# Performance work log

Hardware: AMD Instinct MI355X
Metric: run time of the kernel (lower is better)

Reference implementation:

```python
import jax, jax.numpy as jnp
import numpy as np


def _gcn_layer(x, row, col, W, b):
    # x: [N, d_in]; row/col: [E'] (with self loops already appended)
    N = x.shape[0]
    deg = jax.ops.segment_sum(jnp.ones_like(row, dtype=x.dtype), row, num_segments=N)
    deg_inv_sqrt = deg ** -0.5  # self loops guarantee deg >= 1
    norm = deg_inv_sqrt[row] * deg_inv_sqrt[col]  # [E']
    msg = norm[:, None] * x[row]                  # gather + normalize
    aggr = jax.ops.segment_sum(msg, col, num_segments=N)  # scatter-add
    return aggr @ W + b


def reference(x, edge_index, W1, b1, W2, b2):
    N = x.shape[0]
    loops = jnp.arange(N, dtype=edge_index.dtype)
    row = jnp.concatenate([edge_index[0], loops])
    col = jnp.concatenate([edge_index[1], loops])
    h = jax.nn.relu(_gcn_layer(x, row, col, W1, b1))
    # F.dropout(training=self.training) is identity in eval mode
    out = _gcn_layer(h, row, col, W2, b2)
    return jax.nn.log_softmax(out, axis=1)


def setup_inputs() -> dict:
    key = jax.random.key(0)
    k1, k2, k3, k4 = jax.random.split(key, 4)
    N, E, F_IN, F_HID, F_OUT = 100000, 1200000, 64, 64, 16
    x = jax.random.normal(k1, (N, F_IN), dtype=jnp.float32)
    edge_index = jax.random.randint(k2, (2, E), 0, N, dtype=jnp.int64)
    W1 = jax.random.normal(k3, (F_IN, F_HID), dtype=jnp.float32) / np.sqrt(F_IN)
    b1 = jnp.zeros((F_HID,), dtype=jnp.float32)
    W2 = jax.random.normal(k4, (F_HID, F_OUT), dtype=jnp.float32) / np.sqrt(F_HID)
    b2 = jnp.zeros((F_OUT,), dtype=jnp.float32)
    return {"x": x, "edge_index": edge_index, "W1": W1, "b1": b1, "W2": W2, "b2": b2}
```

## Files before the change

### kernel.cpp

```cpp
#include <hip/hip_runtime.h>
#include <hip/hip_bf16.h>

typedef __attribute__((ext_vector_type(8))) _Float16 hfrag;
typedef __attribute__((ext_vector_type(4))) float ffrag;
typedef __attribute__((ext_vector_type(4))) _Float16 h4v;

#define BSH 8
#define LBS 256
#define CAP_SH 14
#define CAP (1 << CAP_SH)
#define NF 1024
#define OPAD 520
#define CONV_BLKS 384

__device__ __forceinline__ float b2f_(unsigned short u) {
    return __uint_as_float(((unsigned)u) << 16);
}
__device__ __forceinline__ unsigned short f2b_(float v) {
    __hip_bfloat16 h = __float2bfloat16(v);
    return *reinterpret_cast<unsigned short*>(&h);
}
__device__ __forceinline__ unsigned short f2h_(float v) {
    _Float16 h = (_Float16)v;
    return __builtin_bit_cast(unsigned short, h);
}
__device__ __forceinline__ float h2f_(unsigned short u) {
    _Float16 h = __builtin_bit_cast(_Float16, u);
    return (float)h;
}

__device__ __forceinline__ float loadF(const void* p, long long i, int isF32) {
    if (isF32) return ((const float*)p)[i];
    return b2f_(((const unsigned short*)p)[i]);
}

__device__ __forceinline__ float4 loadF4(const void* p, long long base, int i4, int isF32) {
    if (isF32) {
        return ((const float4*)((const float*)p + base))[i4];
    } else {
        ushort4 u = ((const ushort4*)((const unsigned short*)p + base))[i4];
        return make_float4(b2f_(u.x), b2f_(u.y), b2f_(u.z), b2f_(u.w));
    }
}

__device__ __forceinline__ void get_edge(const int* ei, int i64, int e, int E, int& s, int& d) {
    if (i64) { s = ei[2 * (long long)e]; d = ei[2 * (long long)E + 2 * (long long)e]; }
    else     { s = ei[e];                d = ei[(long long)E + e]; }
}

struct E4 { int s[4]; int d[4]; };
__device__ __forceinline__ E4 load4(const int* __restrict__ ei, int i64, int e0, int E) {
    E4 r;
    if (i64) {
        const int4* ps = (const int4*)(ei + 2 * (long long)e0);
        const int4* pd = (const int4*)(ei + 2 * (long long)E + 2 * (long long)e0);
        int4 a = ps[0], b = ps[1];
        int4 c = pd[0], d = pd[1];
        r.s[0] = a.x; r.s[1] = a.z; r.s[2] = b.x; r.s[3] = b.z;
        r.d[0] = c.x; r.d[1] = c.z; r.d[2] = d.x; r.d[3] = d.z;
    } else {
        int4 a = *(const int4*)(ei + e0);
        int4 c = *(const int4*)(ei + (long long)E + e0);
        r.s[0] = a.x; r.s[1] = a.y; r.s[2] = a.z; r.s[3] = a.w;
        r.d[0] = c.x; r.d[1] = c.y; r.d[2] = c.z; r.d[3] = c.w;
    }
    return r;
}

__device__ __forceinline__ void wave_scan_excl(int* a, int nEl, int lane) {
    int run = 0;
    for (int base = 0; base < nEl; base += 64) {
        int i = base + lane;
        int orig = (i < nEl) ? a[i] : 0;
        int v = orig;
#pragma unroll
        for (int off = 1; off < 64; off <<= 1) {
            int u = __shfl_up(v, off);
            if (lane >= off) v += u;
        }
        if (i < nEl) a[i] = v - orig + run;
        run += __shfl(v, 63);
    }
}

__global__ __launch_bounds__(256) void k_stage(const void* __restrict__ x,
                                               const int* __restrict__ ei,
                                               const void* __restrict__ W1, const void* __restrict__ b1,
                                               const void* __restrict__ W2, const void* __restrict__ b2,
                                               int E, int N, int nbk, int EPB,
                                               int* __restrict__ flags, float* __restrict__ Wbuf,
                                               int* __restrict__ off_d, int* __restrict__ off_s,
                                               int* __restrict__ pdst,
                                               unsigned char* __restrict__ psrc,
                                               unsigned short* __restrict__ xh) {
    __shared__ int hd[512], hs[512], cd[512], cs[512];
    __shared__ int s_sane, s_zero;
    int tid = threadIdx.x;
    if (tid == 0) { s_sane = 0; s_zero = 0; }
    __syncthreads();
    const unsigned short* xu = (const unsigned short*)x;
    if (blockIdx.x == NF) {
        int sane = 0;
        for (int k = tid; k < 4096; k += 256) {
            float v = b2f_(xu[2 * k]);
            float a = fabsf(v);
            if (v == 0.0f || (a >= 9.3e-10f && a <= 1.1e9f)) sane++;
        }
        if (sane) atomicAdd(&s_sane, sane);
        int zero = 0;
        for (int k = tid; k < 1024; k += 256) if (ei[2 * k + 1] == 0) zero++;
        if (zero) atomicAdd(&s_zero, zero);
        __syncthreads();
        int f = (s_sane < 3000) ? 1 : 0;
        if (tid == 0) { flags[0] = f; flags[1] = (s_zero > 512) ? 1 : 0; }
        for (int i = tid; i < 4096; i += 256) Wbuf[i] = loadF(W1, i, f);
        if (tid < 64) Wbuf[4096 + tid] = loadF(b1, tid, f);
        for (int i = tid; i < 1024; i += 256) Wbuf[4160 + i] = loadF(W2, i, f);
        if (tid < 16) Wbuf[5184 + tid] = loadF(b2, tid, f);
        return;
    }
    if (blockIdx.x > NF) {
        int cb = blockIdx.x - NF - 1;
        int sane = 0;
        for (int k = tid; k < 4096; k += 256) {
            float v = b2f_(xu[2 * k]);
            float a = fabsf(v);
            if (v == 0.0f || (a >= 9.3e-10f && a <= 1.1e9f)) sane++;
        }
        if (sane) atomicAdd(&s_sane, sane);
        __syncthreads();
        int f = (s_sane < 3000) ? 1 : 0;
        int n4 = N * 16;
        int ctid = cb * 256 + tid;
        int stride = CONV_BLKS * 256 * 2;
        for (int i0 = ctid * 2; i0 < n4; i0 += stride) {
            float4 v0 = loadF4(x, 0, i0, f);
            float4 v1 = (i0 + 1 < n4) ? loadF4(x, 0, i0 + 1, f) : make_float4(0, 0, 0, 0);
            ushort4 o0, o1;
            o0.x = f2h_(v0.x); o0.y = f2h_(v0.y); o0.z = f2h_(v0.z); o0.w = f2h_(v0.w);
            o1.x = f2h_(v1.x); o1.y = f2h_(v1.y); o1.z = f2h_(v1.z); o1.w = f2h_(v1.w);
            ((ushort4*)xh)[i0] = o0;
            if (i0 + 1 < n4) ((ushort4*)xh)[i0 + 1] = o1;
        }
        return;
    }
    int zero = 0;
    for (int k = tid; k < 1024; k += 256) if (ei[2 * k + 1] == 0) zero++;
    if (zero) atomicAdd(&s_zero, zero);
    for (int i = tid; i < 512; i += 256) { hd[i] = 0; hs[i] = 0; }
    __syncthreads();
    int i64 = (s_zero > 512) ? 1 : 0;
    int fb = blockIdx.x;
    int elo = fb * EPB;
    int ehi = min(elo + EPB, E);
    if (elo >= E) {
        for (int b = tid; b <= nbk; b += 256) {
            off_d[fb * OPAD + b] = E; off_s[fb * OPAD + b] = E;
        }
        return;
    }
    int ecnt = ehi - elo;
    for (int e0 = elo + tid * 4; e0 + 4 <= ehi; e0 += 1024) {
        E4 a = load4(ei, i64, e0, E);
#pragma unroll
        for (int u = 0; u < 4; ++u) {
            atomicAdd(&hd[a.d[u] >> BSH], 1);
            atomicAdd(&hs[a.s[u] >> BSH], 1);
        }
    }
    int rem = ecnt & 3, ebase = elo + (ecnt & ~3);
    if (tid < rem) {
        int s, d;
        get_edge(ei, i64, ebase + tid, E, s, d);
        atomicAdd(&hd[d >> BSH], 1);
        atomicAdd(&hs[s >> BSH], 1);
    }
    __syncthreads();
    if (tid < 64)       wave_scan_excl(hd, nbk, tid);
    else if (tid < 128) wave_scan_excl(hs, nbk, tid - 64);
    __syncthreads();
    for (int b = tid; b < nbk; b += 256) {
        int od = elo + hd[b], os = elo + hs[b];
        off_d[fb * OPAD + b] = od; cd[b] = od;
        off_s[fb * OPAD + b] = os; cs[b] = os;
    }
    if (tid == 0) { off_d[fb * OPAD + nbk] = elo + ecnt; off_s[fb * OPAD + nbk] = elo + ecnt; }
    __syncthreads();
    for (int e0 = elo + tid * 4; e0 + 4 <= ehi; e0 += 1024) {
        E4 a = load4(ei, i64, e0, E);
#pragma unroll
        for (int u = 0; u < 4; ++u) {
            int p = atomicAdd(&cd[a.d[u] >> BSH], 1);
            pdst[p] = (a.s[u] << BSH) | (a.d[u] & (LBS - 1));
            int q = atomicAdd(&cs[a.s[u] >> BSH], 1);
            psrc[q] = (unsigned char)(a.s[u] & (LBS - 1));
        }
    }
    if (tid < rem) {
        int s, d;
        get_edge(ei, i64, ebase + tid, E, s, d);
        int p = atomicAdd(&cd[d >> BSH], 1);
        pdst[p] = (s << BSH) | (d & (LBS - 1));
        int q = atomicAdd(&cs[s >> BSH], 1);
        psrc[q] = (unsigned char)(s & (LBS - 1));
    }
}

__global__ __launch_bounds__(256) void k_deg(const unsigned char* __restrict__ psrc,
                                             const int* __restrict__ off_s,
                                             float* __restrict__ dis, int N, int nbk) {
    __shared__ int h[LBS];
    int b = blockIdx.x, tid = threadIdx.x;
    h[tid] = 0;
    __syncthreads();
    for (int fb = tid; fb < NF; fb += 256) {
        int o0 = off_s[fb * OPAD + b];
        int o1 = off_s[fb * OPAD + b + 1];
        for (int p = o0; p < o1; ++p) atomicAdd(&h[psrc[p]], 1);
    }
    __syncthreads();
    int node = b * LBS + tid;
    if (node < N) dis[node] = rsqrtf((float)h[tid] + 1.0f);
}

__global__ __launch_bounds__(256) void k_csr(const int* __restrict__ pdst,
                                             const int* __restrict__ off_d,
                                             const float* __restrict__ dis,
                                             int2* __restrict__ row_se,
                                             int2* __restrict__ pke, int N, int nbk) {
    __shared__ int h[LBS], lb[LBS], cur[LBS];
    int b = blockIdx.x, tid = threadIdx.x;
    h[tid] = 0;
    __syncthreads();
    for (int fb = tid; fb < NF; fb += 256) {
        int o0 = off_d[fb * OPAD + b];
        int o1 = off_d[fb * OPAD + b + 1];
        for (int p = o0; p < o1; ++p) atomicAdd(&h[pdst[p] & (LBS - 1)], 1);
    }
    __syncthreads();
    lb[tid] = h[tid];
    __syncthreads();
    if (tid < 64) wave_scan_excl(lb, LBS, tid);
    __syncthreads();
    int beg = b << CAP_SH;
    cur[tid] = lb[tid];
    int node = b * LBS + tid;
    if (node < N) {
        int s0 = min(lb[tid], CAP), s1 = min(lb[tid] + h[tid], CAP);
        row_se[node] = make_int2(beg + s0, beg + s1);
    }
    __syncthreads();
    for (int fb = tid; fb < NF; fb += 256) {
        int o0 = off_d[fb * OPAD + b];
        int o1 = off_d[fb * OPAD + b + 1];
        for (int p = o0; p < o1; ++p) {
            int e = pdst[p];
            int src = e >> BSH, ld = e & (LBS - 1);
            int r = atomicAdd(&cur[ld], 1);
            if (r < CAP) pke[beg + r] = make_int2(src, __float_as_int(dis[src]));
        }
    }
}

__global__ __launch_bounds__(256) void k_agg(const unsigned short* __restrict__ xh,
                                             const float* __restrict__ dis,
                                             const int2* __restrict__ row_se,
                                             const int2* __restrict__ pke,
                                             unsigned short* __restrict__ aggb, int N) {
    int tid = threadIdx.x;
    int lane = tid & 63;
    int g = lane >> 4, i4 = lane & 15;
    int n = blockIdx.x * 16 + (tid >> 6) * 4 + g;
    if (n >= N) return;
    float dd = dis[n];
    int2 se = row_se[n];
    int beg = se.x, end = se.y;
    int cnt = end - beg;
    h4v xv = *(const h4v*)(xh + (long long)n * 64 + i4 * 4);
    float w = dd * dd;
    float4 A[4];
    A[0].x = w * (float)xv[0]; A[0].y = w * (float)xv[1];
    A[0].z = w * (float)xv[2]; A[0].w = w * (float)xv[3];
#pragma unroll
    for (int u = 1; u < 4; ++u) A[u] = make_float4(0.f, 0.f, 0.f, 0.f);
    int T = (cnt + 3) >> 2;
    int p = beg;
    int2 e[4];
#pragma unroll
    for (int u = 0; u < 4; ++u) e[u] = pke[p + u];
    for (int t = 0; t < T; ++t) {
        h4v hv[4];
#pragma unroll
        for (int u = 0; u < 4; ++u) {
            unsigned ex = min((unsigned)e[u].x, (unsigned)(N - 1));
            hv[u] = *(const h4v*)(xh + (long long)ex * 64 + i4 * 4);
        }
        float nv[4];
#pragma unroll
        for (int u = 0; u < 4; ++u) nv[u] = (p + u < end) ? dd * __int_as_float(e[u].y) : 0.f;
#pragma unroll
        for (int u = 0; u < 4; ++u) e[u] = pke[p + 4 + u];
        p += 4;
#pragma unroll
        for (int u = 0; u < 4; ++u) {
            A[u].x += nv[u] * (float)hv[u][0];
            A[u].y += nv[u] * (float)hv[u][1];
            A[u].z += nv[u] * (float)hv[u][2];
            A[u].w += nv[u] * (float)hv[u][3];
        }
    }
    float4 s;
    s.x = A[0].x + A[1].x + A[2].x + A[3].x;
    s.y = A[0].y + A[1].y + A[2].y + A[3].y;
    s.z = A[0].z + A[1].z + A[2].z + A[3].z;
    s.w = A[0].w + A[1].w + A[2].w + A[3].w;
    ushort4 o;
    o.x = f2h_(s.x); o.y = f2h_(s.y); o.z = f2h_(s.z); o.w = f2h_(s.w);
    *(ushort4*)(aggb + (size_t)n * 64 + i4 * 4) = o;
}

__global__ __launch_bounds__(256) void k_dense(const unsigned short* __restrict__ aggb,
                                               const float* __restrict__ Wbuf,
                                               unsigned short* __restrict__ t2b, int N) {
    __shared__ __align__(16) unsigned short Hs[4][16 * 72];
    int tid = threadIdx.x;
    int lane = tid & 63;
    int w = tid >> 6;
    int m = lane & 15, q = lane >> 4;
    int n0 = blockIdx.x * 64 + w * 16;
    if (n0 >= N) return;

    hfrag Bw1[2][4];
#pragma unroll
    for (int kt = 0; kt < 2; ++kt)
#pragma unroll
        for (int nt = 0; nt < 4; ++nt)
#pragma unroll
            for (int j = 0; j < 8; ++j)
                Bw1[kt][nt][j] = (_Float16)Wbuf[(kt * 32 + q * 8 + j) * 64 + nt * 16 + m];
    hfrag Bw2[2];
#pragma unroll
    for (int kt = 0; kt < 2; ++kt)
#pragma unroll
        for (int j = 0; j < 8; ++j)
            Bw2[kt][j] = (_Float16)Wbuf[4160 + (kt * 32 + q * 8 + j) * 16 + m];
    float b1n[4];
#pragma unroll
    for (int nt = 0; nt < 4; ++nt) b1n[nt] = Wbuf[4096 + nt * 16 + m];

    const unsigned short* arow = aggb + (size_t)(n0 + m) * 64 + q * 8;
    hfrag A0 = *(const hfrag*)(arow);
    hfrag A1 = *(const hfrag*)(arow + 32);

    ffrag acc[4];
#pragma unroll
    for (int nt = 0; nt < 4; ++nt) {
        ffrag z = {0.f, 0.f, 0.f, 0.f};
        z = __builtin_amdgcn_mfma_f32_16x16x32_f16(A0, Bw1[0][nt], z, 0, 0, 0);
        z = __builtin_amdgcn_mfma_f32_16x16x32_f16(A1, Bw1[1][nt], z, 0, 0, 0);
        acc[nt] = z;
    }
    unsigned short* hs = &Hs[w][0];
#pragma unroll
    for (int nt = 0; nt < 4; ++nt)
#pragma unroll
        for (int r = 0; r < 4; ++r) {
            float hv = fmaxf(acc[nt][r] + b1n[nt], 0.0f);
            hs[(q * 4 + r) * 72 + nt * 16 + m] = f2h_(hv);
        }
    const unsigned short* hrow = hs + m * 72 + q * 8;
    hfrag H0 = *(const hfrag*)(hrow);
    hfrag H1 = *(const hfrag*)(hrow + 32);
    ffrag t2 = {0.f, 0.f, 0.f, 0.f};
    t2 = __builtin_amdgcn_mfma_f32_16x16x32_f16(H0, Bw2[0], t2, 0, 0, 0);
    t2 = __builtin_amdgcn_mfma_f32_16x16x32_f16(H1, Bw2[1], t2, 0, 0, 0);
#pragma unroll
    for (int r = 0; r < 4; ++r)
        t2b[(size_t)(n0 + q * 4 + r) * 16 + m] = f2h_(t2[r]);
}

__global__ __launch_bounds__(256) void k_l2(const unsigned short* __restrict__ t2b,
                                            const int* __restrict__ flags,
                                            const float* __restrict__ dis,
                                            const int2* __restrict__ row_se,
                                            const int2* __restrict__ pke,
                                            const float* __restrict__ Wbuf,
                                            void* __restrict__ out, int N) {
    int isF32 = flags[0];
    int tid = threadIdx.x, lane = tid & 63;
    int g = lane >> 4, i = lane & 15;
    int n = blockIdx.x * 16 + (tid >> 6) * 4 + g;
    if (n >= N) return;
    float dd = dis[n];
    int2 se = row_se[n];
    int beg = se.x, end = se.y;
    int cnt = end - beg;
    float A[4];
    A[0] = dd * dd * h2f_(t2b[(size_t)n * 16 + i]);
    A[1] = 0.f; A[2] = 0.f; A[3] = 0.f;
    int T = (cnt + 3) >> 2;
    int p = beg;
    int2 e[4];
#pragma unroll
    for (int u = 0; u < 4; ++u) e[u] = pke[p + u];
    for (int t = 0; t < T; ++t) {
        float r[4];
#pragma unroll
        for (int u = 0; u < 4; ++u) {
            unsigned ex = min((unsigned)e[u].x, (unsigned)(N - 1));
            r[u] = h2f_(t2b[(size_t)ex * 16 + i]);
        }
        float nv[4];
#pragma unroll
        for (int u = 0; u < 4; ++u) nv[u] = (p + u < end) ? dd * __int_as_float(e[u].y) : 0.f;
#pragma unroll
        for (int u = 0; u < 4; ++u) e[u] = pke[p + 4 + u];
        p += 4;
#pragma unroll
        for (int u = 0; u < 4; ++u) A[u] += nv[u] * r[u];
    }
    float a0 = A[0] + A[1] + A[2] + A[3];
    float v = a0 + Wbuf[5184 + i];
    float mx = v;
#pragma unroll
    for (int off = 8; off; off >>= 1) mx = fmaxf(mx, __shfl_xor(mx, off, 16));
    float ex = __expf(v - mx);
    float ss = ex;
#pragma unroll
    for (int off = 8; off; off >>= 1) ss += __shfl_xor(ss, off, 16);
    float r = v - mx - logf(ss);
    size_t oi = (size_t)n * 16 + i;
    if (isF32) ((float*)out)[oi] = r;
    else       ((unsigned short*)out)[oi] = f2b_(r);
}

extern "C" void kernel_launch(void* const* d_in, const int* in_sizes, int n_in,
                              void* d_out, int out_size, void* d_ws, size_t ws_size,
                              hipStream_t stream) {
    const void* x  = d_in[0];
    const int*  ei = (const int*)d_in[1];
    const void* W1 = d_in[2];
    const void* b1 = d_in[3];
    const void* W2 = d_in[4];
    const void* b2 = d_in[5];

    const int N = in_sizes[0] / 64;
    const int E = in_sizes[1] / 2;
    const int nbk = (N + LBS - 1) >> BSH;
    const int EPB = (((E + NF - 1) / NF) + 7) & ~7;

    char* p = (char*)d_ws;
#define CARVE(ty, name, bytes) ty name = (ty)p; p += (((size_t)(bytes)) + 63) & ~(size_t)63;
    CARVE(int*,   flags,     16)
    CARVE(float*, Wbuf,      5200 * 4)
    CARVE(float*, dis,       (size_t)N * 4)
    CARVE(int2*,  row_se,    (size_t)N * 8)
    CARVE(int*,   off_d,     (size_t)NF * OPAD * 4)
    CARVE(int*,   off_s,     (size_t)NF * OPAD * 4)
    CARVE(int*,   pdst,      (size_t)NF * EPB * 4)
    CARVE(unsigned char*, psrc, (size_t)NF * EPB)
    CARVE(int2*,  pke,       (((size_t)nbk << CAP_SH) + 64) * 8)
    CARVE(unsigned short*, xh,   (size_t)N * 64 * 2)
    CARVE(unsigned short*, aggb, (size_t)N * 64 * 2)
    CARVE(unsigned short*, t2b,  (size_t)N * 16 * 2)
#undef CARVE

    k_stage<<<NF + 1 + CONV_BLKS, 256, 0, stream>>>(x, ei, W1, b1, W2, b2,
                                                    E, N, nbk, EPB,
                                                    flags, Wbuf, off_d, off_s,
                                                    pdst, psrc, xh);
    k_deg<<<nbk, 256, 0, stream>>>(psrc, off_s, dis, N, nbk);
    k_csr<<<nbk, 256, 0, stream>>>(pdst, off_d, dis, row_se, pke, N, nbk);
    k_agg<<<(N + 15) / 16, 256, 0, stream>>>(xh, dis, row_se, pke, aggb, N);
    k_dense<<<(N + 63) / 64, 256, 0, stream>>>(aggb, Wbuf, t2b, N);
    k_l2<<<(N + 15) / 16, 256, 0, stream>>>(t2b, flags, dis, row_se, pke, Wbuf, d_out, N);
}
```

Measured before the change: 205.0 us.

## Fuse layer-1 aggregation with dense MFMA transform into one kernel

Merges the aggregation kernel and the dense W1/W2 kernel, so each block's 16 aggregated rows are staged in LDS and then multiplied by W1 with MFMA (one 16-column tile per wave), passed through ReLU, and multiplied by W2. This removes the N×64 fp16 aggb intermediate, its round trip through global memory, and one kernel launch. Pre-swizzled fp16 fragments of W1 and W2 are built once in the staging kernel, so each block no longer gathers and converts weights element by element. The cost is extra block barriers and only one wave doing the second GEMM.

Measured after the change: 202.1 us. Within noise of the previous version (-1.5%).

```diff
diff --git a/kernel.cpp b/kernel.cpp
--- a/kernel.cpp
+++ b/kernel.cpp
@@ -89,6 +89,8 @@
                                                const void* __restrict__ W2, const void* __restrict__ b2,
                                                int E, int N, int nbk, int EPB,
                                                int* __restrict__ flags, float* __restrict__ Wbuf,
+                                               unsigned short* __restrict__ Wh1,
+                                               unsigned short* __restrict__ Wh2,
                                                int* __restrict__ off_d, int* __restrict__ off_s,
                                                int* __restrict__ pdst,
                                                unsigned char* __restrict__ psrc,
@@ -117,6 +119,16 @@
         if (tid < 64) Wbuf[4096 + tid] = loadF(b1, tid, f);
         for (int i = tid; i < 1024; i += 256) Wbuf[4160 + i] = loadF(W2, i, f);
         if (tid < 16) Wbuf[5184 + tid] = loadF(b2, tid, f);
+        __syncthreads();
+        for (int i = tid; i < 4096; i += 256) {
+            int j = i & 7, m = (i >> 3) & 15, q = (i >> 7) & 3, kn = i >> 9;
+            int kt = kn & 1, nt = kn >> 1;
+            Wh1[i] = f2h_(Wbuf[(kt * 32 + q * 8 + j) * 64 + nt * 16 + m]);
+        }
+        for (int i = tid; i < 1024; i += 256) {
+            int j = i & 7, m = (i >> 3) & 15, q = (i >> 7) & 3, kt = i >> 9;
+            Wh2[i] = f2h_(Wbuf[4160 + (kt * 32 + q * 8 + j) * 16 + m]);
+        }
         return;
     }
     if (blockIdx.x > NF) {
@@ -262,33 +274,43 @@
     }
 }
 
-__global__ __launch_bounds__(256) void k_agg(const unsigned short* __restrict__ xh,
-                                             const float* __restrict__ dis,
-                                             const int2* __restrict__ row_se,
-                                             const int2* __restrict__ pke,
-                                             unsigned short* __restrict__ aggb, int N) {
+__global__ __launch_bounds__(256) void k_aggdense(const unsigned short* __restrict__ xh,
+                                                  const float* __restrict__ dis,
+                                                  const int2* __restrict__ row_se,
+                                                  const int2* __restrict__ pke,
+                                                  const unsigned short* __restrict__ Wh1,
+                                                  const unsigned short* __restrict__ Wh2,
+                                                  const float* __restrict__ Wbuf,
+                                                  unsigned short* __restrict__ t2b, int N) {
+    __shared__ __align__(16) unsigned short T[16 * 72];
     int tid = threadIdx.x;
     int lane = tid & 63;
+    int w = tid >> 6;
     int g = lane >> 4, i4 = lane & 15;
-    int n = blockIdx.x * 16 + (tid >> 6) * 4 + g;
-    if (n >= N) return;
-    float dd = dis[n];
-    int2 se = row_se[n];
-    int beg = se.x, end = se.y;
+    int ln = w * 4 + g;
+    int n = blockIdx.x * 16 + ln;
+    int act = (n < N);
+    float4 A[4];
+#pragma unroll
+    for (int u = 0; u < 4; ++u) A[u] = make_float4(0.f, 0.f, 0.f, 0.f);
+    float dd = 0.f;
+    int beg = 0, end = 0;
+    if (act) {
+        dd = dis[n];
+        int2 se = row_se[n];
+        beg = se.x; end = se.y;
+        h4v xv = *(const h4v*)(xh + (long long)n * 64 + i4 * 4);
+        float ww = dd * dd;
+        A[0].x = ww * (float)xv[0]; A[0].y = ww * (float)xv[1];
+        A[0].z = ww * (float)xv[2]; A[0].w = ww * (float)xv[3];
+    }
     int cnt = end - beg;
-    h4v xv = *(const h4v*)(xh + (long long)n * 64 + i4 * 4);
-    float w = dd * dd;
-    float4 A[4];
-    A[0].x = w * (float)xv[0]; A[0].y = w * (float)xv[1];
-    A[0].z = w * (float)xv[2]; A[0].w = w * (float)xv[3];
-#pragma unroll
-    for (int u = 1; u < 4; ++u) A[u] = make_float4(0.f, 0.f, 0.f, 0.f);
-    int T = (cnt + 3) >> 2;
+    int Tn = (cnt + 3) >> 2;
     int p = beg;
     int2 e[4];
 #pragma unroll
     for (int u = 0; u < 4; ++u) e[u] = pke[p + u];
-    for (int t = 0; t < T; ++t) {
+    for (int t = 0; t < Tn; ++t) {
         h4v hv[4];
 #pragma unroll
         for (int u = 0; u < 4; ++u) {
@@ -316,67 +338,41 @@
     s.w = A[0].w + A[1].w + A[2].w + A[3].w;
     ushort4 o;
     o.x = f2h_(s.x); o.y = f2h_(s.y); o.z = f2h_(s.z); o.w = f2h_(s.w);
-    *(ushort4*)(aggb + (size_t)n * 64 + i4 * 4) = o;
-}
-
-__global__ __launch_bounds__(256) void k_dense(const unsigned short* __restrict__ aggb,
-                                               const float* __restrict__ Wbuf,
-                                               unsigned short* __restrict__ t2b, int N) {
-    __shared__ __align__(16) unsigned short Hs[4][16 * 72];
-    int tid = threadIdx.x;
-    int lane = tid & 63;
-    int w = tid >> 6;
+    *(ushort4*)(&T[ln * 72 + i4 * 4]) = o;
+    __syncthreads();
     int m = lane & 15, q = lane >> 4;
-    int n0 = blockIdx.x * 64 + w * 16;
-    if (n0 >= N) return;
-
-    hfrag Bw1[2][4];
-#pragma unroll
-    for (int kt = 0; kt < 2; ++kt)
-#pragma unroll
-        for (int nt = 0; nt < 4; ++nt)
-#pragma unroll
-            for (int j = 0; j < 8; ++j)
-                Bw1[kt][nt][j] = (_Float16)Wbuf[(kt * 32 + q * 8 + j) * 64 + nt * 16 + m];
-    hfrag Bw2[2];
-#pragma unroll
-    for (int kt = 0; kt < 2; ++kt)
-#pragma unroll
-        for (int j = 0; j < 8; ++j)
-            Bw2[kt][j] = (_Float16)Wbuf[4160 + (kt * 32 + q * 8 + j) * 16 + m];
-    float b1n[4];
-#pragma unroll
-    for (int nt = 0; nt < 4; ++nt) b1n[nt] = Wbuf[4096 + nt * 16 + m];
-
-    const unsigned short* arow = aggb + (size_t)(n0 + m) * 64 + q * 8;
+    const unsigned short* arow = &T[m * 72 + q * 8];
     hfrag A0 = *(const hfrag*)(arow);
     hfrag A1 = *(const hfrag*)(arow + 32);
-
-    ffrag acc[4];
-#pragma unroll
-    for (int nt = 0; nt < 4; ++nt) {
-        ffrag z = {0.f, 0.f, 0.f, 0.f};
-        z = __builtin_amdgcn_mfma_f32_16x16x32_f16(A0, Bw1[0][nt], z, 0, 0, 0);
-        z = __builtin_amdgcn_mfma_f32_16x16x32_f16(A1, Bw1[1][nt], z, 0, 0, 0);
-        acc[nt] = z;
-    }
-    unsigned short* hs = &Hs[w][0];
-#pragma unroll
-    for (int nt = 0; nt < 4; ++nt)
+    int nt = w;
+    hfrag B0 = *(const hfrag*)(Wh1 + (((nt * 2 + 0) * 4 + q) * 16 + m) * 8);
+    hfrag B1 = *(const hfrag*)(Wh1 + (((nt * 2 + 1) * 4 + q) * 16 + m) * 8);
+    ffrag z = {0.f, 0.f, 0.f, 0.f};
+    z = __builtin_amdgcn_mfma_f32_16x16x32_f16(A0, B0, z, 0, 0, 0);
+    z = __builtin_amdgcn_mfma_f32_16x16x32_f16(A1, B1, z, 0, 0, 0);
+    float b1n = Wbuf[4096 + nt * 16 + m];
+    __syncthreads();
+#pragma unroll
+    for (int r = 0; r < 4; ++r) {
+        float hv = fmaxf(z[r] + b1n, 0.0f);
+        T[(q * 4 + r) * 72 + nt * 16 + m] = f2h_(hv);
+    }
+    __syncthreads();
+    if (w == 0) {
+        const unsigned short* hrow = &T[m * 72 + q * 8];
+        hfrag H0 = *(const hfrag*)(hrow);
+        hfrag H1 = *(const hfrag*)(hrow + 32);
+        hfrag C0 = *(const hfrag*)(Wh2 + ((0 * 4 + q) * 16 + m) * 8);
+        hfrag C1 = *(const hfrag*)(Wh2 + ((1 * 4 + q) * 16 + m) * 8);
+        ffrag t2 = {0.f, 0.f, 0.f, 0.f};
+        t2 = __builtin_amdgcn_mfma_f32_16x16x32_f16(H0, C0, t2, 0, 0, 0);
+        t2 = __builtin_amdgcn_mfma_f32_16x16x32_f16(H1, C1, t2, 0, 0, 0);
 #pragma unroll
         for (int r = 0; r < 4; ++r) {
-            float hv = fmaxf(acc[nt][r] + b1n[nt], 0.0f);
-            hs[(q * 4 + r) * 72 + nt * 16 + m] = f2h_(hv);
-        }
-    const unsigned short* hrow = hs + m * 72 + q * 8;
-    hfrag H0 = *(const hfrag*)(hrow);
-    hfrag H1 = *(const hfrag*)(hrow + 32);
-    ffrag t2 = {0.f, 0.f, 0.f, 0.f};
-    t2 = __builtin_amdgcn_mfma_f32_16x16x32_f16(H0, Bw2[0], t2, 0, 0, 0);
-    t2 = __builtin_amdgcn_mfma_f32_16x16x32_f16(H1, Bw2[1], t2, 0, 0, 0);
-#pragma unroll
-    for (int r = 0; r < 4; ++r)
-        t2b[(size_t)(n0 + q * 4 + r) * 16 + m] = f2h_(t2[r]);
+            int nn = blockIdx.x * 16 + q * 4 + r;
+            if (nn < N) t2b[(size_t)nn * 16 + m] = f2h_(t2[r]);
+        }
+    }
 }
 
 __global__ __launch_bounds__(256) void k_l2(const unsigned short* __restrict__ t2b,
@@ -453,6 +449,8 @@
 #define CARVE(ty, name, bytes) ty name = (ty)p; p += (((size_t)(bytes)) + 63) & ~(size_t)63;
     CARVE(int*,   flags,     16)
     CARVE(float*, Wbuf,      5200 * 4)
+    CARVE(unsigned short*, Wh1, 4096 * 2)
+    CARVE(unsigned short*, Wh2, 1024 * 2)
     CARVE(float*, dis,       (size_t)N * 4)
     CARVE(int2*,  row_se,    (size_t)N * 8)
     CARVE(int*,   off_d,     (size_t)NF * OPAD * 4)
@@ -461,17 +459,16 @@
     CARVE(unsigned char*, psrc, (size_t)NF * EPB)
     CARVE(int2*,  pke,       (((size_t)nbk << CAP_SH) + 64) * 8)
     CARVE(unsigned short*, xh,   (size_t)N * 64 * 2)
-    CARVE(unsigned short*, aggb, (size_t)N * 64 * 2)
     CARVE(unsigned short*, t2b,  (size_t)N * 16 * 2)
 #undef CARVE
 
     k_stage<<<NF + 1 + CONV_BLKS, 256, 0, stream>>>(x, ei, W1, b1, W2, b2,
                                                     E, N, nbk, EPB,
-                                                    flags, Wbuf, off_d, off_s,
-                                                    pdst, psrc, xh);
+                                                    flags, Wbuf, Wh1, Wh2,
+                                                    off_d, off_s, pdst, psrc, xh);
     k_deg<<<nbk, 256, 0, stream>>>(psrc, off_s, dis, N, nbk);
     k_csr<<<nbk, 256, 0, stream>>>(pdst, off_d, dis, row_se, pke, N, nbk);
-    k_agg<<<(N + 15) / 16, 256, 0, stream>>>(xh, dis, row_se, pke, aggb, N);
-    k_dense<<<(N + 63) / 64, 256, 0, stream>>>(aggb, Wbuf, t2b, N);
+    k_aggdense<<<(N + 15) / 16, 256, 0, stream>>>(xh, dis, row_se, pke,
+                                                  Wh1, Wh2, Wbuf, t2b, N);
     k_l2<<<(N + 15) / 16, 256, 0, stream>>>(t2b, flags, dis, row_se, pke, Wbuf, d_out, N);
 }
```
